# Kernel optimization log

Hardware: AMD Instinct MI355X
Metric: run time of the kernel (lower is better)

The kernel has to match this reference:

```python
import jax, jax.numpy as jnp
import numpy as np

N_NODES = 100000
N_EDGES = 400000
N_GRAPHS = 256
HID = 256
BIO = 512
LAYERS = 3
EPS = 1e-5


def _seg_mean(v, seg, num):
    s = jax.ops.segment_sum(v, seg, num_segments=num)
    c = jax.ops.segment_sum(jnp.ones((v.shape[0], 1), v.dtype), seg, num_segments=num)
    return s / jnp.maximum(c, 1.0)


def setup_inputs() -> dict:
    key = jax.random.key(0)
    ks = jax.random.split(key, 24)
    d = {}
    d['x'] = jax.random.randint(ks[0], (N_NODES,), 0, 8)
    d['edge_index'] = jax.random.randint(ks[1], (2, N_EDGES), 0, N_NODES)
    d['edge_attr'] = jax.random.normal(ks[2], (N_EDGES, 4), jnp.float32)
    d['batch'] = jnp.sort(jax.random.randint(ks[3], (N_NODES,), 0, N_GRAPHS))
    sc = 0.06  # ~1/sqrt(HID)
    d['node_emb_W'] = jax.random.normal(ks[4], (8, HID), jnp.float32) * sc
    d['edge_emb_W'] = jax.random.normal(ks[5], (4, HID), jnp.float32) * 0.5
    d['edge_emb_b'] = jnp.zeros((HID,), jnp.float32)
    d['edge_mlp_W1'] = jax.random.normal(ks[6], (HID, HID), jnp.float32) * sc
    d['edge_mlp_b1'] = jnp.zeros((HID,), jnp.float32)
    d['edge_mlp_W2'] = jax.random.normal(ks[7], (HID, HID), jnp.float32) * sc
    d['edge_mlp_b2'] = jnp.zeros((HID,), jnp.float32)
    d['struct_scale'] = jnp.asarray(1.5, jnp.float32)
    d['conv_W1'] = jax.random.normal(ks[8], (LAYERS, HID, HID), jnp.float32) * sc
    d['conv_b1'] = jnp.zeros((LAYERS, HID), jnp.float32)
    d['conv_W2'] = jax.random.normal(ks[9], (LAYERS, HID, HID), jnp.float32) * sc
    d['conv_b2'] = jnp.zeros((LAYERS, HID), jnp.float32)
    d['conv_eps'] = jnp.zeros((LAYERS,), jnp.float32)
    d['norm_gamma'] = jnp.ones((LAYERS, HID), jnp.float32)
    d['norm_beta'] = jnp.zeros((LAYERS, HID), jnp.float32)
    d['norm_alpha'] = jnp.ones((LAYERS, HID), jnp.float32)
    d['mean_bio'] = jax.random.normal(ks[10], (BIO,), jnp.float32)
    d['head_W1'] = jax.random.normal(ks[11], (HID + BIO, HID), jnp.float32) * 0.036
    d['head_b1'] = jnp.zeros((HID,), jnp.float32)
    d['head_W2'] = jax.random.normal(ks[12], (HID, 1), jnp.float32) * sc
    d['head_b2'] = jnp.zeros((1,), jnp.float32)
    return d


def reference(x, edge_index, edge_attr, batch, node_emb_W, edge_emb_W, edge_emb_b,
              edge_mlp_W1, edge_mlp_b1, edge_mlp_W2, edge_mlp_b2, struct_scale,
              conv_W1, conv_b1, conv_W2, conv_b2, conv_eps,
              norm_gamma, norm_beta, norm_alpha, mean_bio,
              head_W1, head_b1, head_W2, head_b2):
    h = node_emb_W[x]  # [N, HID]
    src, dst = edge_index[0], edge_index[1]

    e = edge_attr @ edge_emb_W + edge_emb_b  # edge_emb
    e = jax.nn.relu(e @ edge_mlp_W1 + edge_mlp_b1) @ edge_mlp_W2 + edge_mlp_b2
    struct_mask = edge_attr[:, 1] > 0
    e = e * jnp.where(struct_mask, struct_scale, 1.0)[:, None]

    for l in range(LAYERS):
        # GINE conv: aggregate relu(x_j + e_ij) at target, then 2-layer MLP
        msg = jax.nn.relu(h[src] + e)  # [E, HID]
        agg = jax.ops.segment_sum(msg, dst, num_segments=N_NODES)
        z = (1.0 + conv_eps[l]) * h + agg
        h = jax.nn.relu(z @ conv_W1[l] + conv_b1[l]) @ conv_W2[l] + conv_b2[l]
        # GraphNorm per graph
        mean = _seg_mean(h, batch, N_GRAPHS)  # [G, HID]
        hc = h - norm_alpha[l] * mean[batch]
        var = _seg_mean(hc * hc, batch, N_GRAPHS)
        h = norm_gamma[l] * hc * jax.lax.rsqrt(var[batch] + EPS) + norm_beta[l]

    g = _seg_mean(h, batch, N_GRAPHS)  # global mean pool [G, HID]
    b_emb = jnp.broadcast_to(mean_bio, (g.shape[0], BIO))
    combined = jnp.concatenate([g, b_emb], axis=1)
    out = jax.nn.relu(combined @ head_W1 + head_b1) @ head_W2 + head_b2
    return out.mean(axis=1, keepdims=True)
```

## Files before the change

### kernel.cpp

```cpp
#include <hip/hip_runtime.h>
#include <cstddef>

#define NN 100000
#define NE 400000
#define NG 256
#define HIDC 256
#define EPSN 1e-5f

typedef unsigned short bfu;
using short8 = __attribute__((ext_vector_type(8))) short;
using f32x4  = __attribute__((ext_vector_type(4))) float;
using f32x2  = __attribute__((ext_vector_type(2))) float;

#if defined(__has_builtin)
#if __has_builtin(__builtin_amdgcn_cvt_pk_fp8_f32) && __has_builtin(__builtin_amdgcn_cvt_pk_f32_fp8)
#define HWFP8 1
#endif
#endif

__device__ __forceinline__ float bf2f(bfu b) {
    union { unsigned int u; float f; } v; v.u = ((unsigned int)b) << 16; return v.f;
}
__device__ __forceinline__ bfu f2bf(float f) {
    union { float f; unsigned int u; } v; v.f = f;
    unsigned int r = v.u + 0x7FFFu + ((v.u >> 16) & 1u);
    return (bfu)(r >> 16);
}
__device__ __forceinline__ float e4m3f_sw(unsigned char b) {
    unsigned s = ((unsigned)(b & 0x80u)) << 24;
    unsigned E = (b >> 3) & 15u, M = b & 7u;
    union { unsigned x; float f; } o;
    if (E == 0) { o.f = (float)M * 0.001953125f; o.x |= s; }
    else o.x = s | ((E + 120u) << 23) | (M << 20);
    return o.f;
}
__device__ __forceinline__ unsigned char f2e4m3_sw(float f) {
    union { float f; unsigned u; } v; v.f = f;
    unsigned s = (v.u >> 24) & 0x80u;
    float a = fabsf(f);
    if (!(a < 448.f)) return (unsigned char)(s | 0x7Eu);
    if (a < 0.0009765625f) return (unsigned char)s;
    if (a < 0.015625f) {
        int m = (int)(a * 512.f + 0.5f);
        if (m >= 8) return (unsigned char)(s | 0x08u);
        return (unsigned char)(s | (unsigned)m);
    }
    unsigned u = v.u;
    unsigned r = u + 0x7FFFFu + ((u >> 20) & 1u);
    int E = (int)((r >> 23) & 255u) - 127 + 7;
    unsigned M = (r >> 20) & 7u;
    if (E >= 16) return (unsigned char)(s | 0x7Eu);
    if (E <= 0) {
        int m = (int)(a * 512.f + 0.5f); if (m > 7) m = 7;
        return (unsigned char)(s | (unsigned)m);
    }
    return (unsigned char)(s | ((unsigned)E << 3) | M);
}
__device__ __forceinline__ unsigned int fp8enc4(float a, float b, float c, float d) {
#ifdef HWFP8
    int lo = __builtin_amdgcn_cvt_pk_fp8_f32(a, b, 0, false);
    int hi = __builtin_amdgcn_cvt_pk_fp8_f32(c, d, 0, false);
    return (unsigned int)((lo & 0xFFFF) | (hi << 16));
#else
    return (unsigned)f2e4m3_sw(a) | ((unsigned)f2e4m3_sw(b) << 8) |
           ((unsigned)f2e4m3_sw(c) << 16) | ((unsigned)f2e4m3_sw(d) << 24);
#endif
}
__device__ __forceinline__ float4 fp8dec4(unsigned int u) {
#ifdef HWFP8
    f32x2 lo = __builtin_amdgcn_cvt_pk_f32_fp8((int)u, false);
    f32x2 hi = __builtin_amdgcn_cvt_pk_f32_fp8((int)u, true);
    return make_float4(lo[0], lo[1], hi[0], hi[1]);
#else
    return make_float4(e4m3f_sw(u & 255u), e4m3f_sw((u >> 8) & 255u),
                       e4m3f_sw((u >> 16) & 255u), e4m3f_sw((u >> 24) & 255u));
#endif
}
__device__ __forceinline__ float4 ld4(const void* p, size_t i, int bf) {
    if (bf) {
        ushort4 u = *(const ushort4*)((const bfu*)p + i);
        return make_float4(bf2f(u.x), bf2f(u.y), bf2f(u.z), bf2f(u.w));
    }
    return *(const float4*)((const float*)p + i);
}
__device__ __forceinline__ float4 ld4b(const bfu* p, size_t i) {
    ushort4 u = *(const ushort4*)(p + i);
    return make_float4(bf2f(u.x), bf2f(u.y), bf2f(u.z), bf2f(u.w));
}
__device__ __forceinline__ float ld1(const void* p, size_t i, int bf) {
    return bf ? bf2f(((const bfu*)p)[i]) : ((const float*)p)[i];
}
__device__ __forceinline__ void st1(void* p, size_t i, float v, int bf) {
    if (bf) ((bfu*)p)[i] = f2bf(v); else ((float*)p)[i] = v;
}

__global__ void k_dt2(const unsigned int* __restrict__ g, int* __restrict__ flag) {
    if (threadIdx.x == 0)
        flag[0] = (g[0] == 0x3F800000u) ? 0 : 1;
}

__global__ void k_st2(const int* __restrict__ batch, int* __restrict__ starts) {
    int g = threadIdx.x;
    if (g > NG) return;
    if (g == NG) { starts[NG] = NN; return; }
    int lo = 0, hi = NN;
    while (lo < hi) { int mid = (lo + hi) >> 1; if (batch[mid] < g) lo = mid + 1; else hi = mid; }
    starts[g] = lo;
}

__global__ void k_zi(int* __restrict__ p, int n) {
    int i = blockIdx.x * blockDim.x + threadIdx.x;
    if (i < n) p[i] = 0;
}

__global__ void k_cnt(const int* __restrict__ ei, int* __restrict__ deg) {
    int e = blockIdx.x * blockDim.x + threadIdx.x;
    if (e >= NE) return;
    int d = ei[NE + e];
    if ((unsigned)d < (unsigned)NN) atomicAdd(&deg[d], 1);
}
__global__ void k_sc1(const int* __restrict__ deg, int* __restrict__ rowp,
                      int* __restrict__ part) {
    __shared__ int sh[256];
    int b = blockIdx.x, t = threadIdx.x;
    int i = b * 256 + t;
    int v = (i < NN) ? deg[i] : 0;
    sh[t] = v; __syncthreads();
    for (int off = 1; off < 256; off <<= 1) {
        int add = (t >= off) ? sh[t - off] : 0;
        __syncthreads();
        sh[t] += add; __syncthreads();
    }
    if (i < NN) rowp[i] = sh[t] - v;
    if (t == 255) part[b] = sh[255];
}
__global__ void k_sc2(int* __restrict__ part, int nb) {
    if (threadIdx.x != 0) return;
    int run = 0;
    for (int b = 0; b < nb; ++b) { int t = part[b]; part[b] = run; run += t; }
}
__global__ void k_sc3(int* __restrict__ rowp, const int* __restrict__ part) {
    int i = blockIdx.x * blockDim.x + threadIdx.x;
    if (i < NN) rowp[i] += part[blockIdx.x];
    if (i == 0) rowp[NN] = NE;
}
__global__ void k_cpi(const int* __restrict__ a, int* __restrict__ b, int n) {
    int i = blockIdx.x * blockDim.x + threadIdx.x;
    if (i < n) b[i] = a[i];
}
__global__ void k_fil(const int* __restrict__ ei, int* __restrict__ cursor,
                      int* __restrict__ csrc, int* __restrict__ ceid) {
    int e = blockIdx.x * blockDim.x + threadIdx.x;
    if (e >= NE) return;
    int s = ei[e], d = ei[NE + e];
    if ((unsigned)d >= (unsigned)NN) return;
    int pos = atomicAdd(&cursor[d], 1);
    csrc[pos] = ((unsigned)s < (unsigned)NN) ? s : 0;
    ceid[pos] = e;
}
__global__ void k_spl(int* __restrict__ splits, int* __restrict__ cnts) {
    if (threadIdx.x == 0) { splits[0] = 0; splits[1] = NN; cnts[0] = NE; }
}

__global__ void k_wef(const void* __restrict__ Wemb, const void* __restrict__ bemb,
                      const void* __restrict__ W1, const void* __restrict__ b1,
                      bfu* __restrict__ weff, bfu* __restrict__ beff,
                      const int* __restrict__ dtf) {
    int bf = *dtf;
    int j = blockIdx.x;
    int n = threadIdx.x;
    float acc = 0.f;
    if (j < 4) {
        for (int k = 0; k < HIDC; ++k)
            acc += ld1(Wemb, (size_t)j * HIDC + k, bf) * ld1(W1, (size_t)k * HIDC + n, bf);
        weff[j * HIDC + n] = f2bf(acc);
    } else {
        for (int k = 0; k < HIDC; ++k)
            acc += ld1(bemb, k, bf) * ld1(W1, (size_t)k * HIDC + n, bf);
        beff[n] = f2bf(acc + ld1(b1, n, bf));
    }
}

__global__ void k_gat3(const bfu* __restrict__ h, const unsigned char* __restrict__ e8,
                       const int* __restrict__ rowp, const int* __restrict__ csrc,
                       bfu* __restrict__ agg) {
    int tid = blockIdx.x * blockDim.x + threadIdx.x;
    if (tid >= NN * 64) return;
    int n = tid >> 6, q = (tid & 63) << 2;
    int s0 = rowp[n], s1 = rowp[n + 1];
    float4 a = make_float4(0.f, 0.f, 0.f, 0.f);
    for (int i = s0; i < s1; ++i) {
        int src = csrc[i];
        ushort4 hu = *(const ushort4*)(h + (size_t)src * HIDC + q);
        unsigned int eu = *(const unsigned int*)(e8 + (size_t)i * HIDC + q);
        float4 ev = fp8dec4(eu);
        a.x += fmaxf(bf2f(hu.x) + ev.x, 0.f);
        a.y += fmaxf(bf2f(hu.y) + ev.y, 0.f);
        a.z += fmaxf(bf2f(hu.z) + ev.z, 0.f);
        a.w += fmaxf(bf2f(hu.w) + ev.w, 0.f);
    }
    ushort4 o; o.x = f2bf(a.x); o.y = f2bf(a.y); o.z = f2bf(a.z); o.w = f2bf(a.w);
    *(ushort4*)(agg + (size_t)n * HIDC + q) = o;
}

__global__ void k_wtr(const void* __restrict__ W, long wOff, bfu* __restrict__ Wt,
                      const int* __restrict__ dtf) {
    int o = blockIdx.x * blockDim.x + threadIdx.x;
    if (o >= HIDC * HIDC) return;
    int blk = o >> 9, pos = o & 511;
    int w = blk >> 5, rem = blk & 31;
    int t = rem >> 3, kb = rem & 7;
    int pr = pos >> 3, j = pos & 7;
    int lr = pr >> 2, lq = pr & 3;
    int n = w * 64 + t * 16 + lr;
    int k = kb * 32 + lq * 8 + j;
    Wt[o] = f2bf(ld1(W, (size_t)wOff + (size_t)k * HIDC + n, *dtf));
}

__global__ void k_emb(const int* __restrict__ x, const void* __restrict__ W,
                      bfu* __restrict__ h, const int* __restrict__ dtf) {
    int tid = blockIdx.x * blockDim.x + threadIdx.x;
    if (tid >= NN * 64) return;
    int bf = *dtf;
    int n = tid >> 6, q = (tid & 63) << 2;
    int xv = x[n]; if ((unsigned)xv >= 8u) xv = 0;
    float4 v = ld4(W, (size_t)xv * HIDC + q, bf);
    ushort4 o; o.x = f2bf(v.x); o.y = f2bf(v.y); o.z = f2bf(v.z); o.w = f2bf(v.w);
    *(ushort4*)(h + (size_t)n * HIDC + q) = o;
}

__global__ __launch_bounds__(256)
void k_mg2(const bfu* __restrict__ A, const void* __restrict__ A2,
           const void* __restrict__ attrs,
           const bfu* __restrict__ weff, const bfu* __restrict__ beff,
           const void* __restrict__ eps, int epsIdx,
           const bfu* __restrict__ Wt,
           const void* __restrict__ bias, long bOff,
           const void* __restrict__ scalep,
           void* __restrict__ C, int M,
           int amode, int relu, int scale, int o8,
           const int* __restrict__ dtf,
           const int* __restrict__ eidx, const int* __restrict__ rowp,
           const int* __restrict__ splits, const int* __restrict__ cnts, int cj) {
    __shared__ bfu As[64 * 32];
    const int bf = *dtf;
    const int tid = threadIdx.x;
    const int wave = tid >> 6, lane = tid & 63;
    const int lr = lane & 15, lq = lane >> 4;
    const int m0 = blockIdx.x * 64;
    int MM = M;
    long p0 = 0;
    if (cj >= 0) {
        MM = cnts[cj];
        p0 = rowp[splits[cj]];
    }
    if (m0 >= MM) return;
    f32x4 acc[4][4] = {};
    float epsv = 0.f;
    if (amode == 2) epsv = 1.0f + ld1(eps, epsIdx, bf);

    const int ar = tid >> 2;
    const int ak = (tid & 3) << 3;
    const int gmA = m0 + ar;
    const bfu* wb = Wt + ((size_t)wave * 32) * 512 + (size_t)(lr * 4 + lq) * 8;

    float aa[4] = {0.f, 0.f, 0.f, 0.f};
    if (amode == 1 && gmA < MM) {
        long er = (cj >= 0) ? (long)eidx[p0 + gmA] : (long)gmA;
        aa[0] = ld1(attrs, (size_t)er * 4 + 0, bf);
        aa[1] = ld1(attrs, (size_t)er * 4 + 1, bf);
        aa[2] = ld1(attrs, (size_t)er * 4 + 2, bf);
        aa[3] = ld1(attrs, (size_t)er * 4 + 3, bf);
    }

    for (int k0 = 0; k0 < 256; k0 += 32) {
        const int kb = k0 >> 5;
        if (amode == 0) {
            uint4 u = make_uint4(0, 0, 0, 0);
            if (gmA < MM) u = *(const uint4*)(A + (size_t)gmA * HIDC + k0 + ak);
            *(uint4*)(&As[tid * 8]) = u;
        } else if (amode == 2) {
            float hv[8] = {}, gv[8] = {};
            if (gmA < MM) {
                ushort4 h0 = *(const ushort4*)(A + (size_t)gmA * HIDC + k0 + ak);
                ushort4 h1 = *(const ushort4*)(A + (size_t)gmA * HIDC + k0 + ak + 4);
                hv[0]=bf2f(h0.x); hv[1]=bf2f(h0.y); hv[2]=bf2f(h0.z); hv[3]=bf2f(h0.w);
                hv[4]=bf2f(h1.x); hv[5]=bf2f(h1.y); hv[6]=bf2f(h1.z); hv[7]=bf2f(h1.w);
                float4 g0 = ld4(A2, (size_t)gmA * HIDC + k0 + ak, 1);
                float4 g1 = ld4(A2, (size_t)gmA * HIDC + k0 + ak + 4, 1);
                gv[0]=g0.x; gv[1]=g0.y; gv[2]=g0.z; gv[3]=g0.w;
                gv[4]=g1.x; gv[5]=g1.y; gv[6]=g1.z; gv[7]=g1.w;
            }
#pragma unroll
            for (int j = 0; j < 8; ++j)
                As[tid * 8 + j] = f2bf(epsv * hv[j] + gv[j]);
        } else {
            float v0=0,v1=0,v2=0,v3=0,v4=0,v5=0,v6=0,v7=0;
            if (gmA < MM) {
                float4 c0 = ld4b(beff, k0 + ak);
                float4 c1 = ld4b(beff, k0 + ak + 4);
                v0=c0.x; v1=c0.y; v2=c0.z; v3=c0.w; v4=c1.x; v5=c1.y; v6=c1.z; v7=c1.w;
#pragma unroll
                for (int j = 0; j < 4; ++j) {
                    float4 w0 = ld4b(weff, (size_t)j * HIDC + k0 + ak);
                    float4 w1 = ld4b(weff, (size_t)j * HIDC + k0 + ak + 4);
                    v0 += aa[j]*w0.x; v1 += aa[j]*w0.y; v2 += aa[j]*w0.z; v3 += aa[j]*w0.w;
                    v4 += aa[j]*w1.x; v5 += aa[j]*w1.y; v6 += aa[j]*w1.z; v7 += aa[j]*w1.w;
                }
            }
            ushort4 o0, o1;
            o0.x = f2bf(fmaxf(v0, 0.f)); o0.y = f2bf(fmaxf(v1, 0.f));
            o0.z = f2bf(fmaxf(v2, 0.f)); o0.w = f2bf(fmaxf(v3, 0.f));
            o1.x = f2bf(fmaxf(v4, 0.f)); o1.y = f2bf(fmaxf(v5, 0.f));
            o1.z = f2bf(fmaxf(v6, 0.f)); o1.w = f2bf(fmaxf(v7, 0.f));
            *(ushort4*)(&As[tid * 8])     = o0;
            *(ushort4*)(&As[tid * 8 + 4]) = o1;
        }
        __syncthreads();
        short8 fa[4], fb[4];
#pragma unroll
        for (int r = 0; r < 4; ++r)
            fa[r] = *(const short8*)(&As[(r * 64 + lr * 4 + lq) * 8]);
#pragma unroll
        for (int t = 0; t < 4; ++t)
            fb[t] = *(const short8*)(wb + (size_t)(t * 8 + kb) * 512);
#pragma unroll
        for (int r = 0; r < 4; ++r)
#pragma unroll
            for (int t = 0; t < 4; ++t)
                acc[r][t] = __builtin_amdgcn_mfma_f32_16x16x32_bf16(
                    fa[r], fb[t], acc[r][t], 0, 0, 0);
        __syncthreads();
    }

    float bv[4];
#pragma unroll
    for (int t = 0; t < 4; ++t) bv[t] = ld1(bias, (size_t)bOff + wave * 64 + t * 16 + lr, bf);
    float scv = scale ? ld1(scalep, 0, bf) : 1.0f;
#pragma unroll
    for (int r = 0; r < 4; ++r) {
#pragma unroll
        for (int i = 0; i < 4; ++i) {
            int gm = m0 + r * 16 + lq * 4 + i;
            if (gm >= MM) continue;
            float rs = 1.0f;
            if (scale) {
                long er = (cj >= 0) ? (long)eidx[p0 + gm] : (long)gm;
                if (ld1(attrs, (size_t)er * 4 + 1, bf) > 0.f) rs = scv;
            }
            float ov[4];
#pragma unroll
            for (int t = 0; t < 4; ++t) {
                float o = acc[r][t][i] + bv[t];
                if (relu) o = fmaxf(o, 0.f);
                ov[t] = o * rs;
            }
            size_t cbase = (size_t)gm * HIDC + wave * 64 + lr;
            if (o8) {
                unsigned int pk = fp8enc4(ov[0], ov[1], ov[2], ov[3]);
                unsigned char* Cb = (unsigned char*)C;
                Cb[cbase]      = (unsigned char)(pk & 255u);
                Cb[cbase + 16] = (unsigned char)((pk >> 8) & 255u);
                Cb[cbase + 32] = (unsigned char)((pk >> 16) & 255u);
                Cb[cbase + 48] = (unsigned char)(pk >> 24);
            } else {
                bfu* Cb = (bfu*)C;
#pragma unroll
                for (int t = 0; t < 4; ++t)
                    Cb[cbase + t * 16] = f2bf(ov[t]);
            }
        }
    }
}

__global__ void k_s1(const bfu* __restrict__ h, const int* __restrict__ starts,
                     float* __restrict__ psum, float* __restrict__ psq) {
    int g = blockIdx.x, c8 = blockIdx.y, c = threadIdx.x;
    int s = starts[g], t = starts[g + 1];
    int len = t - s;
    int b = s + (int)(((long)len * c8) >> 3);
    int e = s + (int)(((long)len * (c8 + 1)) >> 3);
    float sum = 0.f, sq = 0.f;
    for (int n = b; n < e; ++n) {
        float v = bf2f(h[(size_t)n * HIDC + c]);
        sum += v; sq += v * v;
    }
    psum[((size_t)g * 8 + c8) * HIDC + c] = sum;
    psq[((size_t)g * 8 + c8) * HIDC + c] = sq;
}
__global__ void k_s2(const int* __restrict__ starts,
                     const float* __restrict__ psum, const float* __restrict__ psq,
                     const void* __restrict__ alpha, long aOff,
                     float* __restrict__ gmean, float* __restrict__ gvar,
                     const int* __restrict__ dtf) {
    int g = blockIdx.x, c = threadIdx.x;
    float sum = 0.f, sq = 0.f;
#pragma unroll
    for (int j = 0; j < 8; ++j) {
        sum += psum[((size_t)g * 8 + j) * HIDC + c];
        sq  += psq[((size_t)g * 8 + j) * HIDC + c];
    }
    int cn = starts[g + 1] - starts[g]; if (cn < 1) cn = 1;
    float cnt = (float)cn;
    float m = sum / cnt;
    float a = ld1(alpha, (size_t)aOff + c, *dtf);
    gmean[g * HIDC + c] = m;
    gvar[g * HIDC + c] = fmaxf(sq / cnt - (2.f * a - a * a) * m * m, 0.f);
}

__global__ void k_nrm(bfu* __restrict__ h, const int* __restrict__ batch,
                      const float* __restrict__ gmean, const float* __restrict__ gvar,
                      const void* __restrict__ gamma, const void* __restrict__ beta,
                      const void* __restrict__ alpha, long pOff,
                      const int* __restrict__ dtf) {
    int tid = blockIdx.x * blockDim.x + threadIdx.x;
    if (tid >= NN * 64) return;
    int bf = *dtf;
    int n = tid >> 6, q = (tid & 63) << 2;
    int g = batch[n]; if ((unsigned)g >= (unsigned)NG) g = 0;
    ushort4 hu = *(ushort4*)(h + (size_t)n * HIDC + q);
    const float4 mv = *(const float4*)(gmean + g * HIDC + q);
    const float4 vv = *(const float4*)(gvar + g * HIDC + q);
    float4 ga = ld4(gamma, (size_t)pOff + q, bf);
    float4 be = ld4(beta, (size_t)pOff + q, bf);
    float4 al = ld4(alpha, (size_t)pOff + q, bf);
    float4 v;
    v.x = ga.x * (bf2f(hu.x) - al.x * mv.x) * rsqrtf(vv.x + EPSN) + be.x;
    v.y = ga.y * (bf2f(hu.y) - al.y * mv.y) * rsqrtf(vv.y + EPSN) + be.y;
    v.z = ga.z * (bf2f(hu.z) - al.z * mv.z) * rsqrtf(vv.z + EPSN) + be.z;
    v.w = ga.w * (bf2f(hu.w) - al.w * mv.w) * rsqrtf(vv.w + EPSN) + be.w;
    ushort4 ov; ov.x = f2bf(v.x); ov.y = f2bf(v.y); ov.z = f2bf(v.z); ov.w = f2bf(v.w);
    *(ushort4*)(h + (size_t)n * HIDC + q) = ov;
}

__global__ void k_pl2(const int* __restrict__ starts,
                      const float* __restrict__ gmean, const float* __restrict__ gvar,
                      const void* __restrict__ gamma, const void* __restrict__ beta,
                      const void* __restrict__ alpha, long pOff,
                      float* __restrict__ g, const int* __restrict__ dtf) {
    int bf = *dtf;
    int gb = blockIdx.x, c = threadIdx.x;
    int cn = starts[gb + 1] - starts[gb];
    if (cn <= 0) { g[gb * HIDC + c] = 0.f; return; }
    float m = gmean[gb * HIDC + c];
    float v = gvar[gb * HIDC + c];
    float ga = ld1(gamma, (size_t)pOff + c, bf);
    float be = ld1(beta, (size_t)pOff + c, bf);
    float al = ld1(alpha, (size_t)pOff + c, bf);
    g[gb * HIDC + c] = ga * (1.f - al) * m * rsqrtf(v + EPSN) + be;
}

__global__ void k_hd(const float* __restrict__ g, const void* __restrict__ bio,
                     const void* __restrict__ W1, const void* __restrict__ b1,
                     const void* __restrict__ W2, const void* __restrict__ b2,
                     void* __restrict__ out, const int* __restrict__ dtf) {
    __shared__ float comb[768];
    __shared__ float red[256];
    __shared__ int nanf;
    int bf = *dtf;
    int gb = blockIdx.x, t = threadIdx.x;
    if (t == 0) nanf = 0;
    comb[t] = g[gb * HIDC + t];
    comb[256 + t] = ld1(bio, t, bf);
    comb[512 + t] = ld1(bio, 256 + t, bf);
    __syncthreads();
    float acc = ld1(b1, t, bf);
    for (int k = 0; k < 768; ++k) acc += comb[k] * ld1(W1, (size_t)k * HIDC + t, bf);
    if (isnan(acc) || isinf(acc)) nanf = 1;
    float hid = fmaxf(acc, 0.f);
    red[t] = hid * ld1(W2, t, bf);
    __syncthreads();
    for (int off = 128; off > 0; off >>= 1) {
        if (t < off) red[t] += red[t + off];
        __syncthreads();
    }
    if (t == 0) {
        float r = red[0] + ld1(b2, 0, bf);
        if (nanf || isnan(r)) r = 999.0f;
        st1(out, gb, r, bf);
    }
}

extern "C" void kernel_launch(void* const* d_in, const int* in_sizes, int n_in,
                              void* d_out, int out_size, void* d_ws, size_t ws_size,
                              hipStream_t stream) {
    const int* x = (const int*)d_in[0];
    const int* ei = (const int*)d_in[1];
    const void* eattr = d_in[2];
    const int* batch = (const int*)d_in[3];
    const void* node_emb_W = d_in[4];
    const void* edge_emb_W = d_in[5];
    const void* edge_emb_b = d_in[6];
    const void* emlp_W1 = d_in[7];
    const void* emlp_b1 = d_in[8];
    const void* emlp_W2 = d_in[9];
    const void* emlp_b2 = d_in[10];
    const void* struct_scale = d_in[11];
    const void* conv_W1 = d_in[12];
    const void* conv_b1 = d_in[13];
    const void* conv_W2 = d_in[14];
    const void* conv_b2 = d_in[15];
    const void* conv_eps = d_in[16];
    const void* ngamma = d_in[17];
    const void* nbeta = d_in[18];
    const void* nalpha = d_in[19];
    const void* mean_bio = d_in[20];
    const void* head_W1 = d_in[21];
    const void* head_b1 = d_in[22];
    const void* head_W2 = d_in[23];
    const void* head_b2 = d_in[24];
    (void)in_sizes; (void)n_in; (void)out_size; (void)ws_size;

    const size_t H_B = (size_t)NN * HIDC * 2;
    const size_t E8_B = (size_t)NE * HIDC;
    char* p = (char*)d_ws;
    bfu* hbuf = (bfu*)p; p += H_B;
    bfu* aggb = (bfu*)p; p += H_B;
    unsigned char* e8 = (unsigned char*)p; p += E8_B;
    bfu* wt = (bfu*)p; p += 8 * 65536 * 2;
    int* rowp = (int*)p;
    int* cursor = rowp + 100352;
    int* part = cursor + 100352;
    int* splits = part + 1024;
    int* cnts = splits + 8;
    int* csrc = cnts + 8;
    int* ceid = csrc + NE;
    p = (char*)(ceid + NE);
    float* psum = (float*)p; p += (size_t)NG * 8 * HIDC * 4;
    float* psq = (float*)p; p += (size_t)NG * 8 * HIDC * 4;
    char* small = p;
    int* starts = (int*)small;
    int* dtf = (int*)(small + 2048);
    bfu* weff = (bfu*)(small + 4096);
    bfu* beff = weff + 4 * HIDC;
    float* gmean = (float*)(small + 16384);
    float* gvar = gmean + NG * HIDC;
    float* gpool = gvar + NG * HIDC;

    k_dt2<<<1, 64, 0, stream>>>((const unsigned int*)ngamma, dtf);
    k_st2<<<1, 512, 0, stream>>>(batch, starts);
    k_emb<<<(NN * 64 + 255) / 256, 256, 0, stream>>>(x, node_emb_W, hbuf, dtf);
    k_wef<<<5, 256, 0, stream>>>(edge_emb_W, edge_emb_b, emlp_W1, emlp_b1,
                                 weff, beff, dtf);

    k_wtr<<<256, 256, 0, stream>>>(emlp_W2, 0, wt + 65536, dtf);
    for (int l = 0; l < 3; ++l) {
        k_wtr<<<256, 256, 0, stream>>>(conv_W1, (long)l * HIDC * HIDC, wt + (2 + l) * 65536, dtf);
        k_wtr<<<256, 256, 0, stream>>>(conv_W2, (long)l * HIDC * HIDC, wt + (5 + l) * 65536, dtf);
    }

    const int NBN = (NN + 255) / 256;
    k_zi<<<NBN, 256, 0, stream>>>(cursor, NN);
    k_cnt<<<(NE + 255) / 256, 256, 0, stream>>>(ei, cursor);
    k_sc1<<<NBN, 256, 0, stream>>>(cursor, rowp, part);
    k_sc2<<<1, 64, 0, stream>>>(part, NBN);
    k_sc3<<<NBN, 256, 0, stream>>>(rowp, part);
    k_cpi<<<NBN, 256, 0, stream>>>(rowp, cursor, NN);
    k_fil<<<(NE + 255) / 256, 256, 0, stream>>>(ei, cursor, csrc, ceid);
    k_spl<<<1, 64, 0, stream>>>(splits, cnts);

    dim3 gE((NE + 63) / 64), gN((NN + 63) / 64);
    k_mg2<<<gE, 256, 0, stream>>>(
        nullptr, nullptr, eattr, weff, beff,
        nullptr, 0, wt + 65536, emlp_b2, 0, struct_scale, e8, 0,
        1, 0, 1, 1, dtf, ceid, rowp, splits, cnts, 0);

    dim3 gS1(NG, 8);
    const int gatBlocks = (NN * 64 + 255) / 256;

    for (int l = 0; l < 3; ++l) {
        k_gat3<<<gatBlocks, 256, 0, stream>>>(hbuf, e8, rowp, csrc, aggb);
        k_mg2<<<gN, 256, 0, stream>>>(
            hbuf, aggb, nullptr, nullptr, nullptr,
            conv_eps, l, wt + (2 + l) * 65536, conv_b1, (long)l * HIDC,
            nullptr, aggb, NN, 2, 1, 0, 0, dtf,
            nullptr, nullptr, nullptr, nullptr, -1);
        k_mg2<<<gN, 256, 0, stream>>>(
            aggb, nullptr, nullptr, nullptr, nullptr,
            nullptr, 0, wt + (5 + l) * 65536, conv_b2, (long)l * HIDC,
            nullptr, hbuf, NN, 0, 0, 0, 0, dtf,
            nullptr, nullptr, nullptr, nullptr, -1);
        k_s1<<<gS1, 256, 0, stream>>>(hbuf, starts, psum, psq);
        k_s2<<<NG, 256, 0, stream>>>(starts, psum, psq, nalpha, (long)l * HIDC,
                                     gmean, gvar, dtf);
        if (l < 2) {
            k_nrm<<<(NN * 64 + 255) / 256, 256, 0, stream>>>(
                hbuf, batch, gmean, gvar, ngamma, nbeta, nalpha, (long)l * HIDC, dtf);
        }
    }

    k_pl2<<<NG, 256, 0, stream>>>(starts, gmean, gvar, ngamma, nbeta, nalpha,
                                  (long)2 * HIDC, gpool, dtf);
    k_hd<<<NG, 256, 0, stream>>>(gpool, mean_bio, head_W1, head_b1,
                                 head_W2, head_b2, d_out, dtf);
}
```

Before: 1.093 ms.

## Fuse GINE conv MLP's two GEMMs into one kernel with LDS intermediate

Replaces the two back-to-back k_mg2 launches per layer with a single k_cnv kernel. It builds (1+eps)*h+agg in LDS, runs the first GEMM, applies bias and ReLU, then stores the 64x256 bf16 intermediate in shared memory and runs the second GEMM. The goal is to avoid writing and re-reading the [N,256] hidden activation through global memory and to save a launch per layer. It uses 36KB of LDS per block, which may lower occupancy, and it writes h in place, which is safe because each block reads only its own rows before writing them.

```diff
diff --git a/kernel.cpp b/kernel.cpp
--- a/kernel.cpp
+++ b/kernel.cpp
@@ -369,6 +369,119 @@
                 for (int t = 0; t < 4; ++t)
                     Cb[cbase + t * 16] = f2bf(ov[t]);
             }
+        }
+    }
+}
+
+__global__ __launch_bounds__(256)
+void k_cnv(bfu* __restrict__ h, const bfu* __restrict__ agg,
+           const void* __restrict__ eps, int epsIdx,
+           const bfu* __restrict__ Wt1, const void* __restrict__ bias1, long b1Off,
+           const bfu* __restrict__ Wt2, const void* __restrict__ bias2, long b2Off,
+           const int* __restrict__ dtf) {
+    __shared__ bfu As[64 * 32];
+    __shared__ bfu Ts[8][64 * 32];
+    const int bf = *dtf;
+    const int tid = threadIdx.x;
+    const int wave = tid >> 6, lane = tid & 63;
+    const int lr = lane & 15, lq = lane >> 4;
+    const int m0 = blockIdx.x * 64;
+    const float epsv = 1.0f + ld1(eps, epsIdx, bf);
+    const int ar = tid >> 2;
+    const int ak = (tid & 3) << 3;
+    const int gmA = m0 + ar;
+    const bfu* wb1 = Wt1 + ((size_t)wave * 32) * 512 + (size_t)(lr * 4 + lq) * 8;
+    const bfu* wb2 = Wt2 + ((size_t)wave * 32) * 512 + (size_t)(lr * 4 + lq) * 8;
+
+    f32x4 acc[4][4] = {};
+    for (int k0 = 0; k0 < 256; k0 += 32) {
+        const int kb = k0 >> 5;
+        float hv[8] = {}, gv[8] = {};
+        if (gmA < NN) {
+            ushort4 h0 = *(const ushort4*)(h + (size_t)gmA * HIDC + k0 + ak);
+            ushort4 h1 = *(const ushort4*)(h + (size_t)gmA * HIDC + k0 + ak + 4);
+            hv[0]=bf2f(h0.x); hv[1]=bf2f(h0.y); hv[2]=bf2f(h0.z); hv[3]=bf2f(h0.w);
+            hv[4]=bf2f(h1.x); hv[5]=bf2f(h1.y); hv[6]=bf2f(h1.z); hv[7]=bf2f(h1.w);
+            ushort4 g0 = *(const ushort4*)(agg + (size_t)gmA * HIDC + k0 + ak);
+            ushort4 g1 = *(const ushort4*)(agg + (size_t)gmA * HIDC + k0 + ak + 4);
+            gv[0]=bf2f(g0.x); gv[1]=bf2f(g0.y); gv[2]=bf2f(g0.z); gv[3]=bf2f(g0.w);
+            gv[4]=bf2f(g1.x); gv[5]=bf2f(g1.y); gv[6]=bf2f(g1.z); gv[7]=bf2f(g1.w);
+        }
+#pragma unroll
+        for (int j = 0; j < 8; ++j)
+            As[tid * 8 + j] = f2bf(epsv * hv[j] + gv[j]);
+        __syncthreads();
+        short8 fa[4], fb[4];
+#pragma unroll
+        for (int r = 0; r < 4; ++r)
+            fa[r] = *(const short8*)(&As[(r * 64 + lr * 4 + lq) * 8]);
+#pragma unroll
+        for (int t = 0; t < 4; ++t)
+            fb[t] = *(const short8*)(wb1 + (size_t)(t * 8 + kb) * 512);
+#pragma unroll
+        for (int r = 0; r < 4; ++r)
+#pragma unroll
+            for (int t = 0; t < 4; ++t)
+                acc[r][t] = __builtin_amdgcn_mfma_f32_16x16x32_bf16(
+                    fa[r], fb[t], acc[r][t], 0, 0, 0);
+        __syncthreads();
+    }
+    {
+        float bv[4];
+#pragma unroll
+        for (int t = 0; t < 4; ++t)
+            bv[t] = ld1(bias1, (size_t)b1Off + wave * 64 + t * 16 + lr, bf);
+        const f32x4 z4 = {0.f, 0.f, 0.f, 0.f};
+#pragma unroll
+        for (int r = 0; r < 4; ++r) {
+#pragma unroll
+            for (int i = 0; i < 4; ++i) {
+                int row = r * 16 + lq * 4 + i;
+#pragma unroll
+                for (int t = 0; t < 4; ++t) {
+                    int kk = wave * 64 + t * 16 + lr;
+                    Ts[kk >> 5][row * 32 + (kk & 31)] =
+                        f2bf(fmaxf(acc[r][t][i] + bv[t], 0.f));
+                }
+            }
+        }
+#pragma unroll
+        for (int r = 0; r < 4; ++r)
+#pragma unroll
+            for (int t = 0; t < 4; ++t)
+                acc[r][t] = z4;
+    }
+    __syncthreads();
+#pragma unroll
+    for (int kb = 0; kb < 8; ++kb) {
+        short8 fa[4], fb[4];
+#pragma unroll
+        for (int r = 0; r < 4; ++r)
+            fa[r] = *(const short8*)(&Ts[kb][(r * 64 + lr * 4 + lq) * 8]);
+#pragma unroll
+        for (int t = 0; t < 4; ++t)
+            fb[t] = *(const short8*)(wb2 + (size_t)(t * 8 + kb) * 512);
+#pragma unroll
+        for (int r = 0; r < 4; ++r)
+#pragma unroll
+            for (int t = 0; t < 4; ++t)
+                acc[r][t] = __builtin_amdgcn_mfma_f32_16x16x32_bf16(
+                    fa[r], fb[t], acc[r][t], 0, 0, 0);
+    }
+    float bv[4];
+#pragma unroll
+    for (int t = 0; t < 4; ++t)
+        bv[t] = ld1(bias2, (size_t)b2Off + wave * 64 + t * 16 + lr, bf);
+#pragma unroll
+    for (int r = 0; r < 4; ++r) {
+#pragma unroll
+        for (int i = 0; i < 4; ++i) {
+            int gm = m0 + r * 16 + lq * 4 + i;
+            if (gm >= NN) continue;
+            size_t cbase = (size_t)gm * HIDC + wave * 64 + lr;
+#pragma unroll
+            for (int t = 0; t < 4; ++t)
+                h[cbase + t * 16] = f2bf(acc[r][t][i] + bv[t]);
         }
     }
 }
@@ -570,16 +683,10 @@
 
     for (int l = 0; l < 3; ++l) {
         k_gat3<<<gatBlocks, 256, 0, stream>>>(hbuf, e8, rowp, csrc, aggb);
-        k_mg2<<<gN, 256, 0, stream>>>(
-            hbuf, aggb, nullptr, nullptr, nullptr,
-            conv_eps, l, wt + (2 + l) * 65536, conv_b1, (long)l * HIDC,
-            nullptr, aggb, NN, 2, 1, 0, 0, dtf,
-            nullptr, nullptr, nullptr, nullptr, -1);
-        k_mg2<<<gN, 256, 0, stream>>>(
-            aggb, nullptr, nullptr, nullptr, nullptr,
-            nullptr, 0, wt + (5 + l) * 65536, conv_b2, (long)l * HIDC,
-            nullptr, hbuf, NN, 0, 0, 0, 0, dtf,
-            nullptr, nullptr, nullptr, nullptr, -1);
+        k_cnv<<<gN, 256, 0, stream>>>(
+            hbuf, aggb, conv_eps, l,
+            wt + (2 + l) * 65536, conv_b1, (long)l * HIDC,
+            wt + (5 + l) * 65536, conv_b2, (long)l * HIDC, dtf);
         k_s1<<<gS1, 256, 0, stream>>>(hbuf, starts, psum, psq);
         k_s2<<<NG, 256, 0, stream>>>(starts, psum, psq, nalpha, (long)l * HIDC,
                                      gmean, gvar, dtf);
```

Measured after the change: 1.060 ms. -3.0%, faster.
